# Kernel tuning notes

Hardware: AMD Instinct MI355X
Metric: run time of the kernel (lower is better)

The kernel has to match this reference:

```python
import jax, jax.numpy as jnp
import numpy as np

B = 32; N = 512; SEQ_LEN = 8
L = 0.05; T_REF = 5.0; V_TH = 20.0; V_RES = 0.0
SQL = float(np.sqrt(L))
BN_EPS = 1e-5

# ---- Dawson-style lookup tables for the LIF moment activation (built once, float64) ----
_XG = np.linspace(-10.0, 4.0, 7001)
_DX = _XG[1] - _XG[0]

def _cumtrapz(y):
    return np.concatenate([[0.0], np.cumsum(0.5 * (y[1:] + y[:-1]) * _DX)])

_phi = np.exp(-_XG ** 2)
_I = np.exp(-100.0) / 20.0 + _cumtrapz(_phi)          # int_{-inf}^x e^{-t^2} dt (asymptotic tail at -10)
_g = np.exp(_XG ** 2) * _I                             # 1st Dawson-like function g(x)
_G = _cumtrapz(_g)                                     # int g dx (rel. to -10)
_h = np.exp(_XG ** 2) * _cumtrapz(_phi * _g ** 2)      # 2nd Dawson-like function h(x)
_H = _cumtrapz(_h)                                     # int h dx

XG = jnp.asarray(_XG, jnp.float32)
GT = jnp.asarray(_g, jnp.float32)
GI = jnp.asarray(_G, jnp.float32)
HI = jnp.asarray(_H, jnp.float32)

def _interp(x, tab):
    return jnp.interp(x, XG, tab)

def moment_activate(u, s, rho):
    # Mnn_Activate_Mean / Std / Corr: LIF moment activation
    s = jnp.maximum(s, 1e-6)
    ub = jnp.clip((V_TH * L - u) / (s * SQL), -10.0, 4.0)
    lb = jnp.clip((V_RES * L - u) / (s * SQL), -10.0, 4.0)
    dG = _interp(ub, GI) - _interp(lb, GI)
    ua = 1.0 / (T_REF + (2.0 / L) * dG)                               # mean firing rate
    dH = jnp.maximum(_interp(ub, HI) - _interp(lb, HI), 0.0)
    sa = jnp.sqrt((8.0 / L ** 2) * dH * ua ** 3)                      # firing std
    dg = _interp(ub, GT) - _interp(lb, GT)
    chi = ua ** 2 * (2.0 / L) * dg / (SQL * jnp.maximum(sa, 1e-9))    # linear response coeff
    eye = jnp.eye(rho.shape[-1], dtype=rho.dtype)
    rho_out = chi[:, :, None] * chi[:, None, :] * rho                 # [B,N,N]
    rho_out = rho_out * (1.0 - eye) + eye                             # unit diagonal
    return ua, sa, rho_out

def linear_corr(W, b, u, s, rho):
    # Mnn_Linear_Corr: mean via affine map, covariance via W C W^T
    u_out = u @ W.T + b
    Cin = rho * s[:, :, None] * s[:, None, :]                         # [B,N,N] covariance
    C = jnp.einsum('bik,lk->bil', jnp.einsum('ij,bjk->bik', W, Cin), W)
    var = jnp.clip(jnp.diagonal(C, axis1=1, axis2=2), 0.0, None)
    s_out = jnp.sqrt(var)
    denom = s_out[:, :, None] * s_out[:, None, :]
    rho_out = jnp.where(denom > 1e-12, C / jnp.maximum(denom, 1e-12), 0.0)
    return u_out, s_out, rho_out

def mexi_hat(n, k=0.3):
    dx = 2.0 * np.pi / n
    x = np.arange(0.0, 2.0 * np.pi, dx)[:n]
    y = np.exp(2.0 * (np.cos(x) - 1.0)) * np.cos(2.0 * x)
    j = np.arange(n)
    idx = (j[None, :] - j[:, None]) % n                               # w[i,:] = y.roll(i)
    return y[idx].astype(np.float32)

def setup_inputs() -> dict:
    ks = jax.random.split(jax.random.key(0), 10)
    u = jax.random.normal(ks[0], (B, N), jnp.float32)
    s = jax.random.uniform(ks[1], (B, N), jnp.float32, 0.1, 1.0)
    A = jax.random.normal(ks[2], (B, N, N), jnp.float32) / np.sqrt(N)
    sym = 0.5 * (A + jnp.swapaxes(A, 1, 2))
    eye = jnp.eye(N, dtype=jnp.float32)
    rho = jnp.clip(sym, -0.5, 0.5) * (1.0 - eye) + eye                # valid-ish corr matrix
    u_ext = jax.random.normal(ks[3], (B, N), jnp.float32)
    s_ext = jax.random.uniform(ks[4], (B, N), jnp.float32, 0.1, 1.0)
    W = 0.02 * jax.random.normal(ks[5], (N, N), jnp.float32) + 0.1 * jnp.asarray(mexi_hat(N))
    b = 0.02 * jax.random.normal(ks[6], (N,), jnp.float32)
    W_ext = 0.02 * jax.random.normal(ks[7], (N, N), jnp.float32)
    b_ext = 0.02 * jax.random.normal(ks[8], (N,), jnp.float32)
    w_mean = 2.5 * jnp.ones((N,), jnp.float32)
    b_mean = 2.5 * jnp.ones((N,), jnp.float32)
    w_mean_ext = 2.5 * jnp.ones((N,), jnp.float32)
    b_mean_ext = 2.5 * jnp.ones((N,), jnp.float32)
    return {'u': u, 's': s, 'rho': rho, 'u_ext': u_ext, 's_ext': s_ext,
            'W': W, 'b': b, 'W_ext': W_ext, 'b_ext': b_ext,
            'w_mean': w_mean, 'b_mean': b_mean,
            'w_mean_ext': w_mean_ext, 'b_mean_ext': b_mean_ext,
            'seq_len': SEQ_LEN}

def reference(u, s, rho, u_ext, s_ext, W, b, W_ext, b_ext,
              w_mean, b_mean, w_mean_ext, b_mean_ext, seq_len):
    # external pathway (Mnn_Linear_without_Corr + BN), computed once
    u_e = u_ext @ W_ext.T + b_ext
    s_e = jnp.sqrt((s_ext ** 2) @ (W_ext ** 2).T)
    mean_e = jnp.mean(u_e, axis=0); var_e = jnp.var(u_e, axis=0)
    f_e = w_mean_ext / jnp.sqrt(var_e + BN_EPS)
    s_e = s_e * jnp.abs(f_e)                                          # Mnn_Std_Bn1d (uses pre-BN stats)
    u_e = (u_e - mean_e) * f_e + b_mean_ext

    def step(carry, _):
        u, s, rho = carry
        u, s, rho = linear_corr(W, b, u, s, rho)
        mean = jnp.mean(u, axis=0); var = jnp.var(u, axis=0)
        f = w_mean / jnp.sqrt(var + BN_EPS)
        s = s * jnp.abs(f)
        u = (u - mean) * f + b_mean
        u = u + u_e
        s = jnp.sqrt(s * s + s_e * s_e)
        return moment_activate(u, s, rho), None

    (u, s, rho), _ = jax.lax.scan(step, (u, s, rho), None, length=seq_len)
    return u, s, rho
```

## Files before the change

### kernel.cpp

```cpp
#include <hip/hip_runtime.h>
#include <math.h>


#define BB 32
#define NN 512
#define SEQ 8
#define TG 7001
#define SVN (BB * NN)

typedef float f32x4 __attribute__((ext_vector_type(4)));
typedef short s16x8 __attribute__((ext_vector_type(8)));

__device__ __forceinline__ unsigned short bf16_rne(float v) {
    unsigned u = __float_as_uint(v);
    u += 0x7FFFu + ((u >> 16) & 1u);
    return (unsigned short)(u >> 16);
}
__device__ __forceinline__ float bf16_f(unsigned short h) {
    return __uint_as_float(((unsigned)h) << 16);
}
__device__ __forceinline__ void split2(float v, unsigned short& h, unsigned short& l) {
    unsigned short hh = bf16_rne(v);
    h = hh;
    l = bf16_rne(v - bf16_f(hh));
}

__device__ __forceinline__ size_t ts_idx(int r, int k) {
    return (size_t)(((r >> 4) * 16 + (k >> 5)) * 512 + ((k >> 3) & 3) * 128 + (r & 15) * 8 + (k & 7));
}

__device__ __forceinline__ float interp_tab(const float* __restrict__ tab, float x) {
    float t = (x + 10.0f) * 500.0f;
    t = fminf(fmaxf(t, 0.0f), 7000.0f);
    int i0 = (int)t;
    if (i0 > 6999) i0 = 6999;
    float fr = t - (float)i0;
    float a = tab[i0];
    float b = tab[i0 + 1];
    return fmaf(fr, b - a, a);
}

#define GLOAD_LDS16(GP, LP)                                                        \
    __builtin_amdgcn_global_load_lds(                                              \
        (const __attribute__((address_space(1))) unsigned int*)(const void*)(GP),  \
        (__attribute__((address_space(3))) unsigned int*)(void*)(LP), 16, 0, 0)

__global__ void k_exp(double* __restrict__ expP, double* __restrict__ expM) {
    int k = blockIdx.x * 256 + threadIdx.x;
    if (k >= TG) return;
    double x = -10.0 + (14.0 / 7000.0) * k;
    expP[k] = exp(x * x);
    expM[k] = exp(-x * x);
}

__device__ double blk_exscan(double part, double* wsum) {
    int t = threadIdx.x, lane = t & 63, wid = t >> 6;
    double run = part;
    #pragma unroll
    for (int off = 1; off < 64; off <<= 1) {
        double nv = __shfl_up(run, off);
        if (lane >= off) run += nv;
    }
    if (lane == 63) wsum[wid] = run;
    __syncthreads();
    if (t < 16) {
        double v = wsum[t];
        #pragma unroll
        for (int off = 1; off < 16; off <<= 1) {
            double nv = __shfl_up(v, off);
            if (lane >= off) v += nv;
        }
        wsum[t] = v;
    }
    __syncthreads();
    double base = (wid > 0) ? wsum[wid - 1] : 0.0;
    double ex = base + run - part;
    __syncthreads();
    return ex;
}

__global__ __launch_bounds__(1024)
void k_scan(const double* __restrict__ expP, const double* __restrict__ expM,
            float* __restrict__ GT, float* __restrict__ GI, float* __restrict__ HI) {
    __shared__ double ys[7008];
    __shared__ double wsum[16];
    const int t = threadIdx.x;
    const double dx = 14.0 / 7000.0;
    int k0 = t * 7, k1 = k0 + 7;
    if (k1 > TG) k1 = TG;
    if (k0 > TG) k0 = TG;
    int kls = (k0 < 1) ? 1 : k0;

    for (int k = k0; k < k1; ++k) ys[k] = expM[k];
    __syncthreads();

    double tmp[7];
    {
        double part = 0.0;
        for (int k = kls; k < k1; ++k) part += 0.5 * (ys[k - 1] + ys[k]) * dx;
        double run = blk_exscan(part, wsum) + exp(-100.0) / 20.0;
        int c = 0;
        for (int k = k0; k < k1; ++k) {
            if (k >= 1) run += 0.5 * (ys[k - 1] + ys[k]) * dx;
            tmp[c] = expP[k] * run;
            GT[k] = (float)tmp[c];
            ++c;
        }
        __syncthreads();
        c = 0;
        for (int k = k0; k < k1; ++k) ys[k] = tmp[c++];
        __syncthreads();
    }
    {
        double part = 0.0;
        for (int k = kls; k < k1; ++k) part += 0.5 * (ys[k - 1] + ys[k]) * dx;
        double run = blk_exscan(part, wsum);
        for (int k = k0; k < k1; ++k) {
            if (k >= 1) run += 0.5 * (ys[k - 1] + ys[k]) * dx;
            GI[k] = (float)run;
        }
        __syncthreads();
    }
    {
        double part = 0.0;
        for (int k = kls; k < k1; ++k) {
            double ya = expM[k - 1] * ys[k - 1] * ys[k - 1];
            double yb = expM[k] * ys[k] * ys[k];
            part += 0.5 * (ya + yb) * dx;
        }
        double run = blk_exscan(part, wsum);
        int c = 0;
        for (int k = k0; k < k1; ++k) {
            if (k >= 1) {
                double ya = expM[k - 1] * ys[k - 1] * ys[k - 1];
                double yb = expM[k] * ys[k] * ys[k];
                run += 0.5 * (ya + yb) * dx;
            }
            tmp[c++] = run;
        }
        __syncthreads();
        c = 0;
        for (int k = k0; k < k1; ++k) ys[k] = tmp[c++];
        __syncthreads();
    }
    {
        double part = 0.0;
        for (int k = kls; k < k1; ++k)
            part += 0.5 * (expP[k - 1] * ys[k - 1] + expP[k] * ys[k]) * dx;
        double run = blk_exscan(part, wsum);
        for (int k = k0; k < k1; ++k) {
            if (k >= 1) run += 0.5 * (expP[k - 1] * ys[k - 1] + expP[k] * ys[k]) * dx;
            HI[k] = (float)run;
        }
    }
}

__global__ void k_splitW(const float* __restrict__ W,
                         unsigned short* __restrict__ Wh, unsigned short* __restrict__ Wl) {
    int t = blockIdx.x * 256 + threadIdx.x;
    int r = t >> 6, c8 = t & 63;
    int k = c8 * 8;
    const float* src = W + (size_t)r * NN + k;
    s16x8 hv, lv;
    #pragma unroll
    for (int q = 0; q < 8; ++q) {
        unsigned short h, l;
        split2(src[q], h, l);
        hv[q] = (short)h; lv[q] = (short)l;
    }
    size_t o = ts_idx(r, k);
    *reinterpret_cast<s16x8*>(Wh + o) = hv;
    *reinterpret_cast<s16x8*>(Wl + o) = lv;
}

__global__ void k_splitQ(const float* __restrict__ rho, const float* __restrict__ s,
                         unsigned short* __restrict__ Qh, unsigned short* __restrict__ Ql) {
    int t = blockIdx.x * 256 + threadIdx.x;
    int b = t >> 15;
    int rem = t & 32767;
    int r = rem >> 6, c8 = rem & 63;
    int k = c8 * 8;
    const float* src = rho + ((size_t)b * NN + r) * NN + k;
    const float* sb = s + b * NN;
    float si = sb[r];
    s16x8 hv, lv;
    #pragma unroll
    for (int q = 0; q < 8; ++q) {
        float v = src[q] * si * sb[k + q];
        unsigned short h, l;
        split2(v, h, l);
        hv[q] = (short)h; lv[q] = (short)l;
    }
    size_t o = (size_t)b * NN * NN + ts_idx(r, k);
    *reinterpret_cast<s16x8*>(Qh + o) = hv;
    *reinterpret_cast<s16x8*>(Ql + o) = lv;
}

#define MFMAF(AH, AL, BH, BL)                                                  \
    {                                                                          \
        _Pragma("unroll") for (int m_ = 0; m_ < 4; ++m_)                       \
            _Pragma("unroll") for (int n_ = 0; n_ < 2; ++n_)                   \
                acc[m_][n_] = __builtin_amdgcn_mfma_f32_16x16x32_bf16(         \
                    AH[m_], BH[n_], acc[m_][n_], 0, 0, 0);                     \
        _Pragma("unroll") for (int m_ = 0; m_ < 4; ++m_)                       \
            _Pragma("unroll") for (int n_ = 0; n_ < 2; ++n_)                   \
                acc[m_][n_] = __builtin_amdgcn_mfma_f32_16x16x32_bf16(         \
                    AL[m_], BH[n_], acc[m_][n_], 0, 0, 0);                     \
        _Pragma("unroll") for (int m_ = 0; m_ < 4; ++m_)                       \
            _Pragma("unroll") for (int n_ = 0; n_ < 2; ++n_)                   \
                acc[m_][n_] = __builtin_amdgcn_mfma_f32_16x16x32_bf16(         \
                    AH[m_], BL[n_], acc[m_][n_], 0, 0, 0);                     \
    }

#define STAGE(BUFOFF, KB)                                                      \
    {                                                                          \
        _Pragma("unroll") for (int q_ = 0; q_ < 4; ++q_)                       \
            GLOAD_LDS16(gsrc + (size_t)q_ * 8192 + (size_t)(KB) * 512,         \
                        ldst + (BUFOFF) + q_ * 512);                           \
    }

template <int PHASE>
__global__ __launch_bounds__(512, 4)
void gemm_ts(const unsigned short* __restrict__ Ah, const unsigned short* __restrict__ Al,
             long aStride,
             const unsigned short* __restrict__ Bh, const unsigned short* __restrict__ Bl,
             long bStride,
             unsigned short* __restrict__ Oh, unsigned short* __restrict__ Ol,
             float* __restrict__ Of,
             const float* __restrict__ Wf, float* __restrict__ sv,
             const float* __restrict__ u_prev, const float* __restrict__ bvec,
             float* __restrict__ u_linT,
             const float* __restrict__ bn_w, const float* __restrict__ bmv,
             const float* __restrict__ u_e, const float* __restrict__ s_e2,
             const float* __restrict__ GT, const float* __restrict__ GI,
             const float* __restrict__ HI,
             float* __restrict__ u_next, float* __restrict__ s_next) {
    __shared__ __align__(16) unsigned short stg[2 * 16384];
    __shared__ float slS[256], chS[256], snS[256];

    const int id = blockIdx.x;
    const int member = (id >> 3) & 3;
    const int g = (id & 7) | ((id >> 5) << 3);
    const int p = g & 3;
    const int b = g >> 2;
    const int xt = (PHASE == 0) ? p : member;
    const int yt = (PHASE == 0) ? member : p;
    const int i0 = yt * 128, j0 = xt * 128;
    const int tid = threadIdx.x;
    const int w = tid >> 6, lane = tid & 63;
    const int wqm = w >> 2, wqn = w & 3;
    const int laneo = lane * 8;

    const unsigned short* gA_h = Ah + (size_t)b * aStride + (size_t)(i0 >> 4) * 8192 + laneo;
    const unsigned short* gA_l = Al + (size_t)b * aStride + (size_t)(i0 >> 4) * 8192 + laneo;
    const unsigned short* gB_h = Bh + (size_t)b * bStride + (size_t)(j0 >> 4) * 8192 + laneo;
    const unsigned short* gB_l = Bl + (size_t)b * bStride + (size_t)(j0 >> 4) * 8192 + laneo;
    const int arr = w >> 1;
    const unsigned short* gsrc =
        (arr == 0) ? gA_h : (arr == 1) ? gA_l : (arr == 2) ? gB_h : gB_l;
    gsrc += (size_t)((w & 1) * 4) * 8192;
    unsigned short* ldst = stg + (w * 4) * 512;

    STAGE(0, 0);

    if (PHASE == 0) {
        const int tile16 = yt * 4 + xt;
        const int row = tile16 * 32 + (tid >> 4);
        const int seg = tid & 15;
        const float4* wr = (const float4*)(Wf + (size_t)row * NN + seg * 32);
        const float4* ur = (const float4*)(u_prev + b * NN + seg * 32);
        float a0 = 0.f, a1 = 0.f, a2 = 0.f, a3 = 0.f;
        #pragma unroll
        for (int kk = 0; kk < 8; ++kk) {
            float4 wv = wr[kk], uv = ur[kk];
            a0 = fmaf(wv.x, uv.x, a0);
            a1 = fmaf(wv.y, uv.y, a1);
            a2 = fmaf(wv.z, uv.z, a2);
            a3 = fmaf(wv.w, uv.w, a3);
        }
        float au = (a0 + a1) + (a2 + a3);
        au += __shfl_xor(au, 1);
        au += __shfl_xor(au, 2);
        au += __shfl_xor(au, 4);
        au += __shfl_xor(au, 8);
        if (seg == 0) u_linT[row * BB + b] = au + bvec[row];
    } else if (tid < 256) {
        const int ii = (tid < 128) ? (i0 + tid) : (j0 + tid - 128);
        float vb[32];
        {
            const float4* ul = (const float4*)(u_linT + (size_t)ii * BB);
            #pragma unroll
            for (int q = 0; q < 8; ++q) {
                float4 t4 = ul[q];
                vb[q * 4 + 0] = t4.x; vb[q * 4 + 1] = t4.y;
                vb[q * 4 + 2] = t4.z; vb[q * 4 + 3] = t4.w;
            }
        }
        float m = 0.0f;
        #pragma unroll
        for (int bb = 0; bb < BB; ++bb) m += vb[bb];
        m *= (1.0f / BB);
        float v = 0.0f;
        #pragma unroll
        for (int bb = 0; bb < BB; ++bb) {
            float d = vb[bb] - m;
            v = fmaf(d, d, v);
        }
        v *= (1.0f / BB);
        float f = bn_w[ii] / sqrtf(v + 1e-5f);
        const int idx = b * NN + ii;
        float s2;
        {
            const float* svp = sv + idx;
            float q0 = (svp[0 * SVN] + svp[1 * SVN]) + (svp[2 * SVN] + svp[3 * SVN]);
            float q1 = (svp[4 * SVN] + svp[5 * SVN]) + (svp[6 * SVN] + svp[7 * SVN]);
            float q2 = (svp[8 * SVN] + svp[9 * SVN]) + (svp[10 * SVN] + svp[11 * SVN]);
            float q3 = (svp[12 * SVN] + svp[13 * SVN]) + (svp[14 * SVN] + svp[15 * SVN]);
            s2 = (q0 + q1) + (q2 + q3);
        }
        float s_l = sqrtf(fmaxf(s2, 0.0f));
        float un = fmaf(vb[b] - m, f, bmv[ii]) + u_e[idx];
        float sn = sqrtf(fmaf((s_l * s_l) * f, f, s_e2[idx]));
        const float SQL = 0.22360679774997896f;
        float ss = fmaxf(sn, 1e-6f);
        float inv = 1.0f / (ss * SQL);
        float ubx = fminf(fmaxf((1.0f - un) * inv, -10.0f), 4.0f);
        float lbx = fminf(fmaxf((0.0f - un) * inv, -10.0f), 4.0f);
        float dG = interp_tab(GI, ubx) - interp_tab(GI, lbx);
        float ua = 1.0f / fmaf(40.0f, dG, 5.0f);
        float dH = fmaxf(interp_tab(HI, ubx) - interp_tab(HI, lbx), 0.0f);
        float sa = sqrtf(3200.0f * dH * ua * ua * ua);
        float dg2 = interp_tab(GT, ubx) - interp_tab(GT, lbx);
        float ch = ua * ua * 40.0f * dg2 / (SQL * fmaxf(sa, 1e-9f));
        slS[tid] = s_l;
        chS[tid] = ch;
        snS[tid] = sa;
        if (i0 == j0 && tid < 128) {
            u_next[idx] = ua;
            s_next[idx] = sa;
        }
    }

    f32x4 acc[4][2];
    #pragma unroll
    for (int m2 = 0; m2 < 4; ++m2)
        #pragma unroll
        for (int n2 = 0; n2 < 2; ++n2) acc[m2][n2] = (f32x4){0.f, 0.f, 0.f, 0.f};

    __syncthreads();

    #pragma unroll 2
    for (int kb = 0; kb < 16; ++kb) {
        const int cur = (kb & 1) * 16384;
        if (kb < 15) STAGE(16384 - cur, kb + 1);
        const unsigned short* lb = stg + cur;
        s16x8 fah[4], fal[4], fbh[2], fbl[2];
        #pragma unroll
        for (int t = 0; t < 4; ++t) {
            fah[t] = *reinterpret_cast<const s16x8*>(lb + (wqm * 4 + t) * 512 + laneo);
            fal[t] = *reinterpret_cast<const s16x8*>(lb + (8 + wqm * 4 + t) * 512 + laneo);
        }
        #pragma unroll
        for (int t = 0; t < 2; ++t) {
            fbh[t] = *reinterpret_cast<const s16x8*>(lb + (16 + wqn * 2 + t) * 512 + laneo);
            fbl[t] = *reinterpret_cast<const s16x8*>(lb + (24 + wqn * 2 + t) * 512 + laneo);
        }
        MFMAF(fah, fal, fbh, fbl);
        __syncthreads();
    }

    const size_t bofs = (size_t)b * NN * NN;
    const int rb0 = i0 + wqm * 64 + (lane >> 4) * 4;
    const int cb0 = j0 + wqn * 32 + (lane & 15);

    if (PHASE == 0) {
        float dp[16];
        #pragma unroll
        for (int m2 = 0; m2 < 4; ++m2)
            #pragma unroll
            for (int r = 0; r < 4; ++r) {
                int row = rb0 + m2 * 16 + r;
                const float* wrow = Wf + ((size_t)row << 9) + cb0;
                float s = 0.0f;
                #pragma unroll
                for (int n2 = 0; n2 < 2; ++n2) s = fmaf(acc[m2][n2][r], wrow[n2 * 16], s);
                dp[m2 * 4 + r] = s;
            }
        #pragma unroll
        for (int k = 0; k < 16; ++k) {
            #pragma unroll
            for (int off = 1; off < 16; off <<= 1) dp[k] += __shfl_xor(dp[k], off);
        }
        if ((lane & 15) == 0) {
            float* svslot = sv + (size_t)(xt * 4 + wqn) * SVN + b * NN;
            #pragma unroll
            for (int k = 0; k < 16; ++k) {
                int row = rb0 + (k >> 2) * 16 + (k & 3);
                svslot[row] = dp[k];
            }
        }
    }

    if (PHASE == 2) {
        float* fS = (float*)stg + w * 2048;
        #pragma unroll
        for (int m2 = 0; m2 < 4; ++m2)
            #pragma unroll
            for (int r = 0; r < 4; ++r) {
                const int lr = m2 * 16 + (lane >> 4) * 4 + r;
                const float si = slS[wqm * 64 + lr], ci = chS[wqm * 64 + lr];
                const int row = i0 + wqm * 64 + lr;
                #pragma unroll
                for (int n2 = 0; n2 < 2; ++n2) {
                    const int lc = wqn * 32 + n2 * 16 + (lane & 15);
                    const float sj = slS[128 + lc], cj = chS[128 + lc];
                    const int col = j0 + lc;
                    float denom = si * sj;
                    float rv = (denom > 1e-12f) ? (acc[m2][n2][r] / fmaxf(denom, 1e-12f)) : 0.0f;
                    rv *= ci * cj;
                    if (row == col) rv = 1.0f;
                    fS[lr * 32 + n2 * 16 + (lane & 15)] = rv;
                }
            }
        #pragma unroll
        for (int inst = 0; inst < 8; ++inst) {
            const int row = i0 + wqm * 64 + inst * 8 + (lane >> 3);
            const int col = j0 + wqn * 32 + (lane & 7) * 4;
            *reinterpret_cast<f32x4*>(Of + bofs + ((size_t)row << 9) + col) =
                *reinterpret_cast<const f32x4*>(fS + inst * 256 + (lane >> 3) * 32 + (lane & 7) * 4);
        }
    } else {
        unsigned short* hiS = stg + w * 4096;
        unsigned short* loS = hiS + 2048;
        const int laneconst = (((lane & 15) >> 3) << 7) + ((lane >> 4) << 5) + (lane & 7);
        #pragma unroll
        for (int m2 = 0; m2 < 4; ++m2)
            #pragma unroll
            for (int n2 = 0; n2 < 2; ++n2) {
                const int base = laneconst + m2 * 512 + n2 * 256;
                #pragma unroll
                for (int r = 0; r < 4; ++r) {
                    float v;
                    if (PHASE == 0) {
                        v = acc[m2][n2][r];
                    } else {
                        const int lr = wqm * 64 + m2 * 16 + (lane >> 4) * 4 + r;
                        const int lc = wqn * 32 + n2 * 16 + (lane & 15);
                        const float si = slS[lr], ci = chS[lr], qi = snS[lr];
                        const float sj = slS[128 + lc], cj = chS[128 + lc], qj = snS[128 + lc];
                        float denom = si * sj;
                        float rv = (denom > 1e-12f) ? (acc[m2][n2][r] / fmaxf(denom, 1e-12f)) : 0.0f;
                        rv *= ci * cj;
                        if (i0 + lr == j0 + lc) rv = 1.0f;
                        v = rv * qi * qj;
                    }
                    unsigned short h, l;
                    split2(v, h, l);
                    hiS[base + r * 8] = h;
                    loS[base + r * 8] = l;
                }
            }
        #pragma unroll
        for (int lb = 0; lb < 4; ++lb) {
            const int gb = ((i0 >> 4) + wqm * 4 + lb) * 16 + (j0 >> 5) + wqn;
            *reinterpret_cast<s16x8*>(Oh + bofs + (size_t)gb * 512 + laneo) =
                *reinterpret_cast<const s16x8*>(hiS + lb * 512 + laneo);
            *reinterpret_cast<s16x8*>(Ol + bofs + (size_t)gb * 512 + laneo) =
                *reinterpret_cast<const s16x8*>(loS + lb * 512 + laneo);
        }
    }
}

__global__ void k_ext_dots(const float* __restrict__ Wx, const float* __restrict__ bx,
                           const float* __restrict__ ux, const float* __restrict__ sx,
                           float* __restrict__ u_e, float* __restrict__ s_e2) {
    int gw = (blockIdx.x << 2) + (threadIdx.x >> 6);
    int lane = threadIdx.x & 63;
    int b = gw >> 9, i = gw & 511;
    const float* wr = Wx + (size_t)i * NN;
    const float* ub = ux + b * NN;
    const float* sb = sx + b * NN;
    float au = 0.0f, as2 = 0.0f;
    for (int j = lane; j < NN; j += 64) {
        float w = wr[j];
        float s = sb[j];
        au = fmaf(w, ub[j], au);
        as2 = fmaf(w * w, s * s, as2);
    }
    #pragma unroll
    for (int off = 32; off; off >>= 1) {
        au += __shfl_down(au, off);
        as2 += __shfl_down(as2, off);
    }
    if (lane == 0) {
        u_e[b * NN + i] = au + bx[i];
        s_e2[b * NN + i] = as2;
    }
}

__global__ void k_ext_stats(float* __restrict__ u_e, float* __restrict__ s_e2,
                            const float* __restrict__ wmx, const float* __restrict__ bmx) {
    int i = blockIdx.x * blockDim.x + threadIdx.x;
    if (i >= NN) return;
    float m = 0.0f;
    for (int b = 0; b < BB; ++b) m += u_e[b * NN + i];
    m *= (1.0f / BB);
    float v = 0.0f;
    for (int b = 0; b < BB; ++b) {
        float d = u_e[b * NN + i] - m;
        v = fmaf(d, d, v);
    }
    v *= (1.0f / BB);
    float f = wmx[i] / sqrtf(v + 1e-5f);
    float bm = bmx[i];
    for (int b = 0; b < BB; ++b) {
        u_e[b * NN + i] = fmaf(u_e[b * NN + i] - m, f, bm);
        s_e2[b * NN + i] *= f * f;
    }
}

extern "C" void kernel_launch(void* const* d_in, const int* in_sizes, int n_in,
                              void* d_out, int out_size, void* d_ws, size_t ws_size,
                              hipStream_t stream) {
    (void)in_sizes; (void)n_in; (void)out_size; (void)ws_size;
    const float* u_in       = (const float*)d_in[0];
    const float* s_in       = (const float*)d_in[1];
    const float* rho_in     = (const float*)d_in[2];
    const float* u_ext      = (const float*)d_in[3];
    const float* s_ext      = (const float*)d_in[4];
    const float* W          = (const float*)d_in[5];
    const float* bvec       = (const float*)d_in[6];
    const float* W_ext      = (const float*)d_in[7];
    const float* b_ext      = (const float*)d_in[8];
    const float* w_mean     = (const float*)d_in[9];
    const float* b_mean     = (const float*)d_in[10];
    const float* w_mean_ext = (const float*)d_in[11];
    const float* b_mean_ext = (const float*)d_in[12];

    float* out_u   = (float*)d_out;
    float* out_s   = out_u + BB * NN;
    float* out_rho = out_s + BB * NN;
    unsigned short* Qh = (unsigned short*)out_rho;
    unsigned short* Ql = Qh + (size_t)BB * NN * NN;

    char* base = (char*)d_ws;
    size_t off = 0;
    auto alloc = [&](size_t bytes) -> char* {
        char* ptr = base + off;
        off += (bytes + 255) & ~(size_t)255;
        return ptr;
    };
    unsigned short* T1h = (unsigned short*)alloc((size_t)BB * NN * NN * 2);
    unsigned short* T1l = (unsigned short*)alloc((size_t)BB * NN * NN * 2);
    unsigned short* Wh  = (unsigned short*)alloc((size_t)NN * NN * 2);
    unsigned short* Wl  = (unsigned short*)alloc((size_t)NN * NN * 2);
    double* expP = (double*)alloc(TG * 8);
    double* expM = (double*)alloc(TG * 8);
    float* GTt   = (float*)alloc(TG * 4);
    float* GIt   = (float*)alloc(TG * 4);
    float* HIt   = (float*)alloc(TG * 4);
    float* u_e   = (float*)alloc(BB * NN * 4);
    float* s_e2  = (float*)alloc(BB * NN * 4);
    float* uA    = (float*)alloc(BB * NN * 4);
    float* uB2   = (float*)alloc(BB * NN * 4);
    float* sA    = (float*)alloc(BB * NN * 4);
    float* sB2   = (float*)alloc(BB * NN * 4);
    float* u_linT = (float*)alloc(BB * NN * 4);
    float* sv    = (float*)alloc((size_t)16 * BB * NN * 4);

    k_exp<<<28, 256, 0, stream>>>(expP, expM);
    k_scan<<<1, 1024, 0, stream>>>(expP, expM, GTt, GIt, HIt);
    k_splitW<<<128, 256, 0, stream>>>(W, Wh, Wl);
    k_splitQ<<<4096, 256, 0, stream>>>(rho_in, s_in, Qh, Ql);
    k_ext_dots<<<BB * NN / 4, 256, 0, stream>>>(W_ext, b_ext, u_ext, s_ext, u_e, s_e2);
    k_ext_stats<<<2, 256, 0, stream>>>(u_e, s_e2, w_mean_ext, b_mean_ext);

    const float* cu = u_in;

    for (int t = 0; t < SEQ; ++t) {
        gemm_ts<0><<<512, 512, 0, stream>>>(
            Wh, Wl, 0L, Qh, Ql, (long)NN * NN, T1h, T1l, nullptr,
            W, sv, cu, bvec, u_linT,
            nullptr, nullptr, nullptr, nullptr, nullptr, nullptr, nullptr,
            nullptr, nullptr);
        float* nu = (t == SEQ - 1) ? out_u : ((t & 1) ? uA : uB2);
        float* ns = (t == SEQ - 1) ? out_s : ((t & 1) ? sA : sB2);
        if (t < SEQ - 1) {
            gemm_ts<1><<<512, 512, 0, stream>>>(
                T1h, T1l, (long)NN * NN, Wh, Wl, 0L, Qh, Ql, nullptr,
                nullptr, sv, nullptr, nullptr, u_linT,
                w_mean, b_mean, u_e, s_e2, GTt, GIt, HIt, nu, ns);
        } else {
            gemm_ts<2><<<512, 512, 0, stream>>>(
                T1h, T1l, (long)NN * NN, Wh, Wl, 0L, nullptr, nullptr, out_rho,
                nullptr, sv, nullptr, nullptr, u_linT,
                w_mean, b_mean, u_e, s_e2, GTt, GIt, HIt, nu, ns);
        }
        cu = nu;
    }
}
```

Measured before the change: 686.8 us.

## Exploit symmetry of rho in phase-1 GEMM: compute upper-triangle tiles and mirror

The phase-1 GEMM, which produces the next rho/Q operand, now launches only the 10 upper-triangular 128x128 tile pairs per batch instead of all 16. Each off-diagonal tile also writes its transpose through shared memory into the mirrored location. This relies on W C W^T being symmetric to cut matmul work by roughly a third. The cost is an extra LDS transpose pass, two more barriers, and the assumption that the bf16-split result stays exactly symmetric.

```diff
diff --git a/kernel.cpp b/kernel.cpp
--- a/kernel.cpp
+++ b/kernel.cpp
@@ -239,12 +239,22 @@
     __shared__ float slS[256], chS[256], snS[256];
 
     const int id = blockIdx.x;
-    const int member = (id >> 3) & 3;
-    const int g = (id & 7) | ((id >> 5) << 3);
-    const int p = g & 3;
-    const int b = g >> 2;
-    const int xt = (PHASE == 0) ? p : member;
-    const int yt = (PHASE == 0) ? member : p;
+    int xt, yt, b;
+    if (PHASE == 1) {
+        const int pair = id % 10;
+        b = id / 10;
+        if (pair < 4)      { yt = 0; xt = pair; }
+        else if (pair < 7) { yt = 1; xt = pair - 3; }
+        else if (pair < 9) { yt = 2; xt = pair - 5; }
+        else               { yt = 3; xt = 3; }
+    } else {
+        const int member = (id >> 3) & 3;
+        const int g = (id & 7) | ((id >> 5) << 3);
+        const int p = g & 3;
+        b = g >> 2;
+        xt = (PHASE == 0) ? p : member;
+        yt = (PHASE == 0) ? member : p;
+    }
     const int i0 = yt * 128, j0 = xt * 128;
     const int tid = threadIdx.x;
     const int w = tid >> 6, lane = tid & 63;
@@ -430,14 +440,11 @@
                 *reinterpret_cast<const f32x4*>(fS + inst * 256 + (lane >> 3) * 32 + (lane & 7) * 4);
         }
     } else {
-        unsigned short* hiS = stg + w * 4096;
-        unsigned short* loS = hiS + 2048;
-        const int laneconst = (((lane & 15) >> 3) << 7) + ((lane >> 4) << 5) + (lane & 7);
+        unsigned hl[4][2][4];
         #pragma unroll
         for (int m2 = 0; m2 < 4; ++m2)
             #pragma unroll
-            for (int n2 = 0; n2 < 2; ++n2) {
-                const int base = laneconst + m2 * 512 + n2 * 256;
+            for (int n2 = 0; n2 < 2; ++n2)
                 #pragma unroll
                 for (int r = 0; r < 4; ++r) {
                     float v;
@@ -456,8 +463,20 @@
                     }
                     unsigned short h, l;
                     split2(v, h, l);
-                    hiS[base + r * 8] = h;
-                    loS[base + r * 8] = l;
+                    hl[m2][n2][r] = (unsigned)h | ((unsigned)l << 16);
+                }
+        unsigned short* hiS = stg + w * 4096;
+        unsigned short* loS = hiS + 2048;
+        const int laneconst = (((lane & 15) >> 3) << 7) + ((lane >> 4) << 5) + (lane & 7);
+        #pragma unroll
+        for (int m2 = 0; m2 < 4; ++m2)
+            #pragma unroll
+            for (int n2 = 0; n2 < 2; ++n2) {
+                const int base = laneconst + m2 * 512 + n2 * 256;
+                #pragma unroll
+                for (int r = 0; r < 4; ++r) {
+                    hiS[base + r * 8] = (unsigned short)(hl[m2][n2][r] & 0xFFFFu);
+                    loS[base + r * 8] = (unsigned short)(hl[m2][n2][r] >> 16);
                 }
             }
         #pragma unroll
@@ -467,6 +486,31 @@
                 *reinterpret_cast<const s16x8*>(hiS + lb * 512 + laneo);
             *reinterpret_cast<s16x8*>(Ol + bofs + (size_t)gb * 512 + laneo) =
                 *reinterpret_cast<const s16x8*>(loS + lb * 512 + laneo);
+        }
+        if (PHASE == 1 && yt != xt) {
+            __syncthreads();
+            #pragma unroll
+            for (int m2 = 0; m2 < 4; ++m2)
+                #pragma unroll
+                for (int n2 = 0; n2 < 2; ++n2)
+                    #pragma unroll
+                    for (int r = 0; r < 4; ++r) {
+                        const int rowp = wqn * 32 + n2 * 16 + (lane & 15);
+                        const int colp = wqm * 64 + m2 * 16 + (lane >> 4) * 4 + r;
+                        const int off = ((rowp >> 4) * 4 + (colp >> 5)) * 512 +
+                                        ((colp >> 3) & 3) * 128 + (rowp & 15) * 8 + (colp & 7);
+                        stg[off] = (unsigned short)(hl[m2][n2][r] & 0xFFFFu);
+                        stg[16384 + off] = (unsigned short)(hl[m2][n2][r] >> 16);
+                    }
+            __syncthreads();
+            #pragma unroll
+            for (int cb = 0; cb < 4; ++cb) {
+                const int gb = ((j0 >> 4) + w) * 16 + (i0 >> 5) + cb;
+                *reinterpret_cast<s16x8*>(Oh + bofs + (size_t)gb * 512 + laneo) =
+                    *reinterpret_cast<const s16x8*>(stg + (w * 4 + cb) * 512 + laneo);
+                *reinterpret_cast<s16x8*>(Ol + bofs + (size_t)gb * 512 + laneo) =
+                    *reinterpret_cast<const s16x8*>(stg + 16384 + (w * 4 + cb) * 512 + laneo);
+            }
         }
     }
 }
@@ -586,7 +630,7 @@
         float* nu = (t == SEQ - 1) ? out_u : ((t & 1) ? uA : uB2);
         float* ns = (t == SEQ - 1) ? out_s : ((t & 1) ? sA : sB2);
         if (t < SEQ - 1) {
-            gemm_ts<1><<<512, 512, 0, stream>>>(
+            gemm_ts<1><<<320, 512, 0, stream>>>(
                 T1h, T1l, (long)NN * NN, Wh, Wl, 0L, Qh, Ql, nullptr,
                 nullptr, sv, nullptr, nullptr, u_linT,
                 w_mean, b_mean, u_e, s_e2, GTt, GIt, HIt, nu, ns);
```

Result: slower. 703.8 us (+2.5%).

## Enlarge GEMM tile to 256x128 with 1024 threads and triple-buffered async staging

Applied to the files above, without the earlier changes.

Each block now computes a 256x128 output tile with 16 waves instead of 128x128 with 8 waves, halving the grid and increasing B-operand reuse per block. LDS staging moves from double to triple buffering, with explicit vmcnt waits and a single barrier per k-step so global-to-LDS loads run two stages ahead. The per-row statistics arrays and the epilogue indexing are resized to match. The cost is more LDS per block (about 144 KB of staging) and larger blocks, which likely limits residency to one block per CU and reduces parallelism with only 256 blocks.

```diff
diff --git a/kernel.cpp b/kernel.cpp
--- a/kernel.cpp
+++ b/kernel.cpp
@@ -7,6 +7,7 @@
 #define SEQ 8
 #define TG 7001
 #define SVN (BB * NN)
+#define BUFW 24576
 
 typedef float f32x4 __attribute__((ext_vector_type(4)));
 typedef short s16x8 __attribute__((ext_vector_type(8)));
@@ -212,15 +213,8 @@
                     AH[m_], BL[n_], acc[m_][n_], 0, 0, 0);                     \
     }
 
-#define STAGE(BUFOFF, KB)                                                      \
-    {                                                                          \
-        _Pragma("unroll") for (int q_ = 0; q_ < 4; ++q_)                       \
-            GLOAD_LDS16(gsrc + (size_t)q_ * 8192 + (size_t)(KB) * 512,         \
-                        ldst + (BUFOFF) + q_ * 512);                           \
-    }
-
 template <int PHASE>
-__global__ __launch_bounds__(512, 4)
+__global__ __launch_bounds__(1024, 4)
 void gemm_ts(const unsigned short* __restrict__ Ah, const unsigned short* __restrict__ Al,
              long aStride,
              const unsigned short* __restrict__ Bh, const unsigned short* __restrict__ Bl,
@@ -235,37 +229,42 @@
              const float* __restrict__ GT, const float* __restrict__ GI,
              const float* __restrict__ HI,
              float* __restrict__ u_next, float* __restrict__ s_next) {
-    __shared__ __align__(16) unsigned short stg[2 * 16384];
-    __shared__ float slS[256], chS[256], snS[256];
+    __shared__ __align__(16) unsigned short stg[3 * BUFW];
+    __shared__ float slS[384], chS[384], snS[384];
 
     const int id = blockIdx.x;
-    const int member = (id >> 3) & 3;
-    const int g = (id & 7) | ((id >> 5) << 3);
-    const int p = g & 3;
-    const int b = g >> 2;
-    const int xt = (PHASE == 0) ? p : member;
-    const int yt = (PHASE == 0) ? member : p;
-    const int i0 = yt * 128, j0 = xt * 128;
+    const int b = id >> 3;
+    const int combo = id & 7;
+    const int yt = combo >> 2;
+    const int xt = combo & 3;
+    const int i0 = yt * 256, j0 = xt * 128;
     const int tid = threadIdx.x;
     const int w = tid >> 6, lane = tid & 63;
     const int wqm = w >> 2, wqn = w & 3;
     const int laneo = lane * 8;
 
-    const unsigned short* gA_h = Ah + (size_t)b * aStride + (size_t)(i0 >> 4) * 8192 + laneo;
-    const unsigned short* gA_l = Al + (size_t)b * aStride + (size_t)(i0 >> 4) * 8192 + laneo;
-    const unsigned short* gB_h = Bh + (size_t)b * bStride + (size_t)(j0 >> 4) * 8192 + laneo;
-    const unsigned short* gB_l = Bl + (size_t)b * bStride + (size_t)(j0 >> 4) * 8192 + laneo;
-    const int arr = w >> 1;
-    const unsigned short* gsrc =
-        (arr == 0) ? gA_h : (arr == 1) ? gA_l : (arr == 2) ? gB_h : gB_l;
-    gsrc += (size_t)((w & 1) * 4) * 8192;
-    unsigned short* ldst = stg + (w * 4) * 512;
-
-    STAGE(0, 0);
+    const int c0 = w * 3;
+    const unsigned short* gp[3];
+    #pragma unroll
+    for (int q = 0; q < 3; ++q) {
+        const int c = c0 + q;
+        const unsigned short* src;
+        if (c < 16)      src = Ah + (size_t)b * aStride + (size_t)((i0 >> 4) + c) * 8192;
+        else if (c < 32) src = Al + (size_t)b * aStride + (size_t)((i0 >> 4) + c - 16) * 8192;
+        else if (c < 40) src = Bh + (size_t)b * bStride + (size_t)((j0 >> 4) + c - 32) * 8192;
+        else             src = Bl + (size_t)b * bStride + (size_t)((j0 >> 4) + c - 40) * 8192;
+        gp[q] = src + laneo;
+    }
+    auto STAGEQ = [&](int buf, int kb) {
+        #pragma unroll
+        for (int q = 0; q < 3; ++q)
+            GLOAD_LDS16(gp[q] + (size_t)kb * 512, stg + buf * BUFW + (c0 + q) * 512);
+    };
+
+    STAGEQ(0, 0);
 
     if (PHASE == 0) {
-        const int tile16 = yt * 4 + xt;
-        const int row = tile16 * 32 + (tid >> 4);
+        const int row = combo * 64 + (tid >> 4);
         const int seg = tid & 15;
         const float4* wr = (const float4*)(Wf + (size_t)row * NN + seg * 32);
         const float4* ur = (const float4*)(u_prev + b * NN + seg * 32);
@@ -284,8 +283,8 @@
         au += __shfl_xor(au, 4);
         au += __shfl_xor(au, 8);
         if (seg == 0) u_linT[row * BB + b] = au + bvec[row];
-    } else if (tid < 256) {
-        const int ii = (tid < 128) ? (i0 + tid) : (j0 + tid - 128);
+    } else if (tid < 384) {
+        const int ii = (tid < 256) ? (i0 + tid) : (j0 + tid - 256);
         float vb[32];
         {
             const float4* ul = (const float4*)(u_linT + (size_t)ii * BB);
@@ -335,7 +334,7 @@
         slS[tid] = s_l;
         chS[tid] = ch;
         snS[tid] = sa;
-        if (i0 == j0 && tid < 128) {
+        if (yt == 0 && tid >= 256) {
             u_next[idx] = ua;
             s_next[idx] = sa;
         }
@@ -347,26 +346,37 @@
         #pragma unroll
         for (int n2 = 0; n2 < 2; ++n2) acc[m2][n2] = (f32x4){0.f, 0.f, 0.f, 0.f};
 
-    __syncthreads();
-
-    #pragma unroll 2
+    STAGEQ(1, 1);
+    asm volatile("s_waitcnt vmcnt(3)" ::: "memory");
+    __builtin_amdgcn_sched_barrier(0);
+    __builtin_amdgcn_s_barrier();
+    __builtin_amdgcn_sched_barrier(0);
+
+    #pragma unroll
     for (int kb = 0; kb < 16; ++kb) {
-        const int cur = (kb & 1) * 16384;
-        if (kb < 15) STAGE(16384 - cur, kb + 1);
-        const unsigned short* lb = stg + cur;
+        const int cur = kb % 3;
+        if (kb < 14) STAGEQ((kb + 2) % 3, kb + 2);
+        const unsigned short* lbuf = stg + cur * BUFW;
         s16x8 fah[4], fal[4], fbh[2], fbl[2];
         #pragma unroll
         for (int t = 0; t < 4; ++t) {
-            fah[t] = *reinterpret_cast<const s16x8*>(lb + (wqm * 4 + t) * 512 + laneo);
-            fal[t] = *reinterpret_cast<const s16x8*>(lb + (8 + wqm * 4 + t) * 512 + laneo);
+            fah[t] = *reinterpret_cast<const s16x8*>(lbuf + (wqm * 4 + t) * 512 + laneo);
+            fal[t] = *reinterpret_cast<const s16x8*>(lbuf + (16 + wqm * 4 + t) * 512 + laneo);
         }
         #pragma unroll
         for (int t = 0; t < 2; ++t) {
-            fbh[t] = *reinterpret_cast<const s16x8*>(lb + (16 + wqn * 2 + t) * 512 + laneo);
-            fbl[t] = *reinterpret_cast<const s16x8*>(lb + (24 + wqn * 2 + t) * 512 + laneo);
+            fbh[t] = *reinterpret_cast<const s16x8*>(lbuf + (32 + wqn * 2 + t) * 512 + laneo);
+            fbl[t] = *reinterpret_cast<const s16x8*>(lbuf + (40 + wqn * 2 + t) * 512 + laneo);
         }
         MFMAF(fah, fal, fbh, fbl);
-        __syncthreads();
+        if (kb < 14) {
+            asm volatile("s_waitcnt vmcnt(3)" ::: "memory");
+        } else if (kb == 14) {
+            asm volatile("s_waitcnt vmcnt(0)" ::: "memory");
+        }
+        __builtin_amdgcn_sched_barrier(0);
+        __builtin_amdgcn_s_barrier();
+        __builtin_amdgcn_sched_barrier(0);
     }
 
     const size_t bofs = (size_t)b * NN * NN;
@@ -413,7 +423,7 @@
                 #pragma unroll
                 for (int n2 = 0; n2 < 2; ++n2) {
                     const int lc = wqn * 32 + n2 * 16 + (lane & 15);
-                    const float sj = slS[128 + lc], cj = chS[128 + lc];
+                    const float sj = slS[256 + lc], cj = chS[256 + lc];
                     const int col = j0 + lc;
                     float denom = si * sj;
                     float rv = (denom > 1e-12f) ? (acc[m2][n2][r] / fmaxf(denom, 1e-12f)) : 0.0f;
@@ -447,7 +457,7 @@
                         const int lr = wqm * 64 + m2 * 16 + (lane >> 4) * 4 + r;
                         const int lc = wqn * 32 + n2 * 16 + (lane & 15);
                         const float si = slS[lr], ci = chS[lr], qi = snS[lr];
-                        const float sj = slS[128 + lc], cj = chS[128 + lc], qj = snS[128 + lc];
+                        const float sj = slS[256 + lc], cj = chS[256 + lc], qj = snS[256 + lc];
                         float denom = si * sj;
                         float rv = (denom > 1e-12f) ? (acc[m2][n2][r] / fmaxf(denom, 1e-12f)) : 0.0f;
                         rv *= ci * cj;
@@ -461,12 +471,12 @@
                 }
             }
         #pragma unroll
-        for (int lb = 0; lb < 4; ++lb) {
-            const int gb = ((i0 >> 4) + wqm * 4 + lb) * 16 + (j0 >> 5) + wqn;
+        for (int lb_ = 0; lb_ < 4; ++lb_) {
+            const int gb = ((i0 >> 4) + wqm * 4 + lb_) * 16 + (j0 >> 5) + wqn;
             *reinterpret_cast<s16x8*>(Oh + bofs + (size_t)gb * 512 + laneo) =
-                *reinterpret_cast<const s16x8*>(hiS + lb * 512 + laneo);
+                *reinterpret_cast<const s16x8*>(hiS + lb_ * 512 + laneo);
             *reinterpret_cast<s16x8*>(Ol + bofs + (size_t)gb * 512 + laneo) =
-                *reinterpret_cast<const s16x8*>(loS + lb * 512 + laneo);
+                *reinterpret_cast<const s16x8*>(loS + lb_ * 512 + laneo);
         }
     }
 }
@@ -578,7 +588,7 @@
     const float* cu = u_in;
 
     for (int t = 0; t < SEQ; ++t) {
-        gemm_ts<0><<<512, 512, 0, stream>>>(
+        gemm_ts<0><<<256, 1024, 0, stream>>>(
             Wh, Wl, 0L, Qh, Ql, (long)NN * NN, T1h, T1l, nullptr,
             W, sv, cu, bvec, u_linT,
             nullptr, nullptr, nullptr, nullptr, nullptr, nullptr, nullptr,
@@ -586,12 +596,12 @@
         float* nu = (t == SEQ - 1) ? out_u : ((t & 1) ? uA : uB2);
         float* ns = (t == SEQ - 1) ? out_s : ((t & 1) ? sA : sB2);
         if (t < SEQ - 1) {
-            gemm_ts<1><<<512, 512, 0, stream>>>(
+            gemm_ts<1><<<256, 1024, 0, stream>>>(
                 T1h, T1l, (long)NN * NN, Wh, Wl, 0L, Qh, Ql, nullptr,
                 nullptr, sv, nullptr, nullptr, u_linT,
                 w_mean, b_mean, u_e, s_e2, GTt, GIt, HIt, nu, ns);
         } else {
-            gemm_ts<2><<<512, 512, 0, stream>>>(
+            gemm_ts<2><<<256, 1024, 0, stream>>>(
                 T1h, T1l, (long)NN * NN, Wh, Wl, 0L, nullptr, nullptr, out_rho,
                 nullptr, sv, nullptr, nullptr, u_linT,
                 w_mean, b_mean, u_e, s_e2, GTt, GIt, HIt, nu, ns);
```

Measured after the change: 787.5 us. +14.7%, slower.

## Stage only one operand in LDS, load the other directly from global

Applied to the files above, without the earlier changes.

The GEMM kernel now stages only one operand (B in phase 0, A in other phases) into shared memory through the double buffer, and each wave reads its private operand fragments straight from global memory. This halves the staging buffer. The epilogues are restructured into two passes so they fit in the smaller LDS, which is meant to raise occupancy and cut LDS traffic. In exchange, per-wave global loads sit on the critical path without prefetch, which may expose memory latency.

```diff
diff --git a/kernel.cpp b/kernel.cpp
--- a/kernel.cpp
+++ b/kernel.cpp
@@ -206,17 +206,20 @@
             _Pragma("unroll") for (int n_ = 0; n_ < 2; ++n_)                   \
                 acc[m_][n_] = __builtin_amdgcn_mfma_f32_16x16x32_bf16(         \
                     AL[m_], BH[n_], acc[m_][n_], 0, 0, 0);                     \
-        _Pragma("unroll") for (int m_ = 0; m_ < 4; ++m_)                       \
+        _Pragma("unroll") for (int m_ = 0; m_ < 2; ++m_)                       \
             _Pragma("unroll") for (int n_ = 0; n_ < 2; ++n_)                   \
                 acc[m_][n_] = __builtin_amdgcn_mfma_f32_16x16x32_bf16(         \
                     AH[m_], BL[n_], acc[m_][n_], 0, 0, 0);                     \
-    }
-
-#define STAGE(BUFOFF, KB)                                                      \
-    {                                                                          \
-        _Pragma("unroll") for (int q_ = 0; q_ < 4; ++q_)                       \
-            GLOAD_LDS16(gsrc + (size_t)q_ * 8192 + (size_t)(KB) * 512,         \
-                        ldst + (BUFOFF) + q_ * 512);                           \
+        _Pragma("unroll") for (int m_ = 2; m_ < 4; ++m_)                       \
+            _Pragma("unroll") for (int n_ = 0; n_ < 2; ++n_)                   \
+                acc[m_][n_] = __builtin_amdgcn_mfma_f32_16x16x32_bf16(         \
+                    AH[m_], BL[n_], acc[m_][n_], 0, 0, 0);                     \
+    }
+
+#define STAGE(BUFOFF, KB)                                                          \
+    {                                                                              \
+        GLOAD_LDS16(gp[0] + (size_t)(KB) * 512, stg + (BUFOFF) + (c0 + 0) * 512);  \
+        GLOAD_LDS16(gp[1] + (size_t)(KB) * 512, stg + (BUFOFF) + (c0 + 1) * 512);  \
     }
 
 template <int PHASE>
@@ -235,7 +238,7 @@
              const float* __restrict__ GT, const float* __restrict__ GI,
              const float* __restrict__ HI,
              float* __restrict__ u_next, float* __restrict__ s_next) {
-    __shared__ __align__(16) unsigned short stg[2 * 16384];
+    __shared__ __align__(16) unsigned short stg[2 * 8192];
     __shared__ float slS[256], chS[256], snS[256];
 
     const int id = blockIdx.x;
@@ -251,15 +254,35 @@
     const int wqm = w >> 2, wqn = w & 3;
     const int laneo = lane * 8;
 
-    const unsigned short* gA_h = Ah + (size_t)b * aStride + (size_t)(i0 >> 4) * 8192 + laneo;
-    const unsigned short* gA_l = Al + (size_t)b * aStride + (size_t)(i0 >> 4) * 8192 + laneo;
-    const unsigned short* gB_h = Bh + (size_t)b * bStride + (size_t)(j0 >> 4) * 8192 + laneo;
-    const unsigned short* gB_l = Bl + (size_t)b * bStride + (size_t)(j0 >> 4) * 8192 + laneo;
-    const int arr = w >> 1;
-    const unsigned short* gsrc =
-        (arr == 0) ? gA_h : (arr == 1) ? gA_l : (arr == 2) ? gB_h : gB_l;
-    gsrc += (size_t)((w & 1) * 4) * 8192;
-    unsigned short* ldst = stg + (w * 4) * 512;
+    const int c0 = w * 2;
+    const unsigned short* gp[2];
+    #pragma unroll
+    for (int q = 0; q < 2; ++q) {
+        const int c = c0 + q;
+        if (PHASE == 0) {
+            gp[q] = ((c < 8) ? Bh + (size_t)b * bStride + (size_t)((j0 >> 4) + c) * 8192
+                             : Bl + (size_t)b * bStride + (size_t)((j0 >> 4) + c - 8) * 8192) + laneo;
+        } else {
+            gp[q] = ((c < 8) ? Ah + (size_t)b * aStride + (size_t)((i0 >> 4) + c) * 8192
+                             : Al + (size_t)b * aStride + (size_t)((i0 >> 4) + c - 8) * 8192) + laneo;
+        }
+    }
+
+    const unsigned short* pdh[4];
+    const unsigned short* pdl[4];
+    if (PHASE == 0) {
+        #pragma unroll
+        for (int t = 0; t < 4; ++t) {
+            pdh[t] = Ah + (size_t)b * aStride + (size_t)((i0 >> 4) + wqm * 4 + t) * 8192 + laneo;
+            pdl[t] = Al + (size_t)b * aStride + (size_t)((i0 >> 4) + wqm * 4 + t) * 8192 + laneo;
+        }
+    } else {
+        #pragma unroll
+        for (int t = 0; t < 2; ++t) {
+            pdh[t] = Bh + (size_t)b * bStride + (size_t)((j0 >> 4) + wqn * 2 + t) * 8192 + laneo;
+            pdl[t] = Bl + (size_t)b * bStride + (size_t)((j0 >> 4) + wqn * 2 + t) * 8192 + laneo;
+        }
+    }
 
     STAGE(0, 0);
 
@@ -351,19 +374,32 @@
 
     #pragma unroll 2
     for (int kb = 0; kb < 16; ++kb) {
-        const int cur = (kb & 1) * 16384;
-        if (kb < 15) STAGE(16384 - cur, kb + 1);
+        const int cur = (kb & 1) * 8192;
+        if (kb < 15) STAGE(8192 - cur, kb + 1);
         const unsigned short* lb = stg + cur;
         s16x8 fah[4], fal[4], fbh[2], fbl[2];
-        #pragma unroll
-        for (int t = 0; t < 4; ++t) {
-            fah[t] = *reinterpret_cast<const s16x8*>(lb + (wqm * 4 + t) * 512 + laneo);
-            fal[t] = *reinterpret_cast<const s16x8*>(lb + (8 + wqm * 4 + t) * 512 + laneo);
-        }
-        #pragma unroll
-        for (int t = 0; t < 2; ++t) {
-            fbh[t] = *reinterpret_cast<const s16x8*>(lb + (16 + wqn * 2 + t) * 512 + laneo);
-            fbl[t] = *reinterpret_cast<const s16x8*>(lb + (24 + wqn * 2 + t) * 512 + laneo);
+        if (PHASE == 0) {
+            #pragma unroll
+            for (int t = 0; t < 4; ++t) {
+                fah[t] = *reinterpret_cast<const s16x8*>(pdh[t] + (size_t)kb * 512);
+                fal[t] = *reinterpret_cast<const s16x8*>(pdl[t] + (size_t)kb * 512);
+            }
+            #pragma unroll
+            for (int t = 0; t < 2; ++t) {
+                fbh[t] = *reinterpret_cast<const s16x8*>(lb + (wqn * 2 + t) * 512 + laneo);
+                fbl[t] = *reinterpret_cast<const s16x8*>(lb + (8 + wqn * 2 + t) * 512 + laneo);
+            }
+        } else {
+            #pragma unroll
+            for (int t = 0; t < 4; ++t) {
+                fah[t] = *reinterpret_cast<const s16x8*>(lb + (wqm * 4 + t) * 512 + laneo);
+                fal[t] = *reinterpret_cast<const s16x8*>(lb + (8 + wqm * 4 + t) * 512 + laneo);
+            }
+            #pragma unroll
+            for (int t = 0; t < 2; ++t) {
+                fbh[t] = *reinterpret_cast<const s16x8*>(pdh[t] + (size_t)kb * 512);
+                fbl[t] = *reinterpret_cast<const s16x8*>(pdl[t] + (size_t)kb * 512);
+            }
         }
         MFMAF(fah, fal, fbh, fbl);
         __syncthreads();
@@ -402,71 +438,77 @@
     }
 
     if (PHASE == 2) {
-        float* fS = (float*)stg + w * 2048;
-        #pragma unroll
-        for (int m2 = 0; m2 < 4; ++m2)
-            #pragma unroll
-            for (int r = 0; r < 4; ++r) {
-                const int lr = m2 * 16 + (lane >> 4) * 4 + r;
-                const float si = slS[wqm * 64 + lr], ci = chS[wqm * 64 + lr];
-                const int row = i0 + wqm * 64 + lr;
-                #pragma unroll
-                for (int n2 = 0; n2 < 2; ++n2) {
-                    const int lc = wqn * 32 + n2 * 16 + (lane & 15);
-                    const float sj = slS[128 + lc], cj = chS[128 + lc];
-                    const int col = j0 + lc;
-                    float denom = si * sj;
-                    float rv = (denom > 1e-12f) ? (acc[m2][n2][r] / fmaxf(denom, 1e-12f)) : 0.0f;
-                    rv *= ci * cj;
-                    if (row == col) rv = 1.0f;
-                    fS[lr * 32 + n2 * 16 + (lane & 15)] = rv;
-                }
-            }
-        #pragma unroll
-        for (int inst = 0; inst < 8; ++inst) {
-            const int row = i0 + wqm * 64 + inst * 8 + (lane >> 3);
-            const int col = j0 + wqn * 32 + (lane & 7) * 4;
-            *reinterpret_cast<f32x4*>(Of + bofs + ((size_t)row << 9) + col) =
-                *reinterpret_cast<const f32x4*>(fS + inst * 256 + (lane >> 3) * 32 + (lane & 7) * 4);
-        }
-    } else {
-        unsigned short* hiS = stg + w * 4096;
-        unsigned short* loS = hiS + 2048;
-        const int laneconst = (((lane & 15) >> 3) << 7) + ((lane >> 4) << 5) + (lane & 7);
-        #pragma unroll
-        for (int m2 = 0; m2 < 4; ++m2)
-            #pragma unroll
-            for (int n2 = 0; n2 < 2; ++n2) {
-                const int base = laneconst + m2 * 512 + n2 * 256;
+        float* fS = (float*)stg + w * 1024;
+        #pragma unroll
+        for (int pass = 0; pass < 2; ++pass) {
+            #pragma unroll
+            for (int m2h = 0; m2h < 2; ++m2h) {
+                const int m2 = pass * 2 + m2h;
                 #pragma unroll
                 for (int r = 0; r < 4; ++r) {
-                    float v;
-                    if (PHASE == 0) {
-                        v = acc[m2][n2][r];
-                    } else {
-                        const int lr = wqm * 64 + m2 * 16 + (lane >> 4) * 4 + r;
+                    const int lr = m2 * 16 + (lane >> 4) * 4 + r;
+                    const int lrl = m2h * 16 + (lane >> 4) * 4 + r;
+                    const float si = slS[wqm * 64 + lr], ci = chS[wqm * 64 + lr];
+                    const int row = i0 + wqm * 64 + lr;
+                    #pragma unroll
+                    for (int n2 = 0; n2 < 2; ++n2) {
                         const int lc = wqn * 32 + n2 * 16 + (lane & 15);
-                        const float si = slS[lr], ci = chS[lr], qi = snS[lr];
-                        const float sj = slS[128 + lc], cj = chS[128 + lc], qj = snS[128 + lc];
+                        const float sj = slS[128 + lc], cj = chS[128 + lc];
+                        const int col = j0 + lc;
                         float denom = si * sj;
                         float rv = (denom > 1e-12f) ? (acc[m2][n2][r] / fmaxf(denom, 1e-12f)) : 0.0f;
                         rv *= ci * cj;
-                        if (i0 + lr == j0 + lc) rv = 1.0f;
-                        v = rv * qi * qj;
+                        if (row == col) rv = 1.0f;
+                        fS[lrl * 32 + n2 * 16 + (lane & 15)] = rv;
                     }
-                    unsigned short h, l;
-                    split2(v, h, l);
-                    hiS[base + r * 8] = h;
-                    loS[base + r * 8] = l;
                 }
             }
-        #pragma unroll
-        for (int lb = 0; lb < 4; ++lb) {
-            const int gb = ((i0 >> 4) + wqm * 4 + lb) * 16 + (j0 >> 5) + wqn;
-            *reinterpret_cast<s16x8*>(Oh + bofs + (size_t)gb * 512 + laneo) =
-                *reinterpret_cast<const s16x8*>(hiS + lb * 512 + laneo);
-            *reinterpret_cast<s16x8*>(Ol + bofs + (size_t)gb * 512 + laneo) =
-                *reinterpret_cast<const s16x8*>(loS + lb * 512 + laneo);
+            #pragma unroll
+            for (int inst = 0; inst < 4; ++inst) {
+                const int row = i0 + wqm * 64 + pass * 32 + inst * 8 + (lane >> 3);
+                const int col = j0 + wqn * 32 + (lane & 7) * 4;
+                *reinterpret_cast<f32x4*>(Of + bofs + ((size_t)row << 9) + col) =
+                    *reinterpret_cast<const f32x4*>(fS + inst * 256 + (lane >> 3) * 32 + (lane & 7) * 4);
+            }
+        }
+    } else {
+        unsigned short* rS = stg + w * 2048;
+        const int laneconst = (((lane & 15) >> 3) << 7) + ((lane >> 4) << 5) + (lane & 7);
+        #pragma unroll
+        for (int pass = 0; pass < 2; ++pass) {
+            #pragma unroll
+            for (int m2 = 0; m2 < 4; ++m2)
+                #pragma unroll
+                for (int n2 = 0; n2 < 2; ++n2) {
+                    const int base = laneconst + m2 * 512 + n2 * 256;
+                    #pragma unroll
+                    for (int r = 0; r < 4; ++r) {
+                        float v;
+                        if (PHASE == 0) {
+                            v = acc[m2][n2][r];
+                        } else {
+                            const int lr = wqm * 64 + m2 * 16 + (lane >> 4) * 4 + r;
+                            const int lc = wqn * 32 + n2 * 16 + (lane & 15);
+                            const float si = slS[lr], ci = chS[lr], qi = snS[lr];
+                            const float sj = slS[128 + lc], cj = chS[128 + lc], qj = snS[128 + lc];
+                            float denom = si * sj;
+                            float rv = (denom > 1e-12f) ? (acc[m2][n2][r] / fmaxf(denom, 1e-12f)) : 0.0f;
+                            rv *= ci * cj;
+                            if (i0 + lr == j0 + lc) rv = 1.0f;
+                            v = rv * qi * qj;
+                        }
+                        unsigned short h, l;
+                        split2(v, h, l);
+                        rS[base + r * 8] = (pass == 0) ? h : l;
+                    }
+                }
+            unsigned short* dst = (pass == 0) ? Oh : Ol;
+            #pragma unroll
+            for (int lb_ = 0; lb_ < 4; ++lb_) {
+                const int gb = ((i0 >> 4) + wqm * 4 + lb_) * 16 + (j0 >> 5) + wqn;
+                *reinterpret_cast<s16x8*>(dst + bofs + (size_t)gb * 512 + laneo) =
+                    *reinterpret_cast<const s16x8*>(rS + lb_ * 512 + laneo);
+            }
         }
     }
 }
```

After: 817.4 us. 1.19x slower.
